# Optimization experiments

Measured on AMD Instinct MI355X. Metric: run time of the kernel, lower is better.

Reference implementation:

```python
import jax, jax.numpy as jnp
import numpy as np

# Static multi-scale feature map shapes (value_spatial_shapes) - constants for jit.
SPATIAL = [(128, 128), (64, 64), (32, 32), (16, 16)]
D = 256      # embed_dim
NH = 8       # num_heads
HD = D // NH # head_dim = 32
L = 4        # num_levels
P = 4        # num_points
TP = NH * L * P  # 128 total points


def setup_inputs() -> dict:
    key = jax.random.key(0)
    ks = jax.random.split(key, 10)
    bs, lq = 8, 300
    lv = sum(h * w for h, w in SPATIAL)  # 21760
    s = D ** -0.5
    return {
        "query": jax.random.normal(ks[0], (bs, lq, D), jnp.float32),
        "reference_points": jax.random.uniform(ks[1], (bs, lq, L, 4), jnp.float32),
        "value": jax.random.normal(ks[2], (bs, lv, D), jnp.float32),
        "W_value": jax.random.normal(ks[3], (D, D), jnp.float32) * s,
        "b_value": jnp.zeros((D,), jnp.float32),
        "W_off": jax.random.normal(ks[4], (D, TP * 2), jnp.float32) * (s * 0.01),
        "b_off": jax.random.normal(ks[5], (TP * 2,), jnp.float32) * 0.5,
        "W_attn": jax.random.normal(ks[6], (D, TP), jnp.float32) * (s * 0.01),
        "b_attn": jnp.zeros((TP,), jnp.float32),
        "W_out": jax.random.normal(ks[7], (D, D), jnp.float32) * s,
        "b_out": jnp.zeros((D,), jnp.float32),
    }


def _grid_sample(img, grid):
    """torch F.grid_sample(mode='bilinear', padding_mode='zeros', align_corners=False).
    img: [N, C, H, W]; grid: [N, Hg, Wg, 2] in [-1, 1] (x, y). Returns [N, C, Hg, Wg]."""
    N, C, H, W = img.shape
    gx = (grid[..., 0] + 1.0) * (W * 0.5) - 0.5
    gy = (grid[..., 1] + 1.0) * (H * 0.5) - 0.5
    x0f = jnp.floor(gx)
    y0f = jnp.floor(gy)
    x0 = x0f.astype(jnp.int32)
    y0 = y0f.astype(jnp.int32)
    x1, y1 = x0 + 1, y0 + 1
    wx1 = gx - x0f
    wy1 = gy - y0f
    wx0 = 1.0 - wx1
    wy0 = 1.0 - wy1
    imgf = img.reshape(N, C, H * W)

    def gather(ix, iy):
        valid = (ix >= 0) & (ix < W) & (iy >= 0) & (iy < H)
        idx = jnp.clip(iy, 0, H - 1) * W + jnp.clip(ix, 0, W - 1)
        v = jax.vmap(lambda im, ii: im[:, ii])(imgf, idx)  # [N, C, Hg, Wg]
        return v * valid[:, None, :, :].astype(img.dtype)

    return (gather(x0, y0) * (wx0 * wy0)[:, None]
            + gather(x1, y0) * (wx1 * wy0)[:, None]
            + gather(x0, y1) * (wx0 * wy1)[:, None]
            + gather(x1, y1) * (wx1 * wy1)[:, None])


def reference(query, reference_points, value, W_value, b_value, W_off, b_off,
              W_attn, b_attn, W_out, b_out):
    bs, lq, _ = query.shape
    # value projection + head split
    v = (value @ W_value + b_value).reshape(bs, -1, NH, HD)
    # sampling offsets and attention weights from query
    off = (query @ W_off + b_off).reshape(bs, lq, NH, L, P, 2)
    aw = jax.nn.softmax((query @ W_attn + b_attn).reshape(bs, lq, NH, L * P), axis=-1)
    aw = aw.reshape(bs, lq, NH, L, P)
    # reference_points last dim == 4 branch (cx, cy, w, h)
    ref = reference_points  # [bs, lq, L, 4]
    loc = ref[:, :, None, :, None, :2] + off / P * ref[:, :, None, :, None, 2:] * 0.5
    grids = 2.0 * loc - 1.0  # [bs, lq, NH, L, P, 2]
    # split value per level
    splits = np.cumsum([h * w for h, w in SPATIAL])[:-1]
    v_list = jnp.split(v, splits, axis=1)
    samples = []
    for l, (h, w) in enumerate(SPATIAL):
        img = v_list[l].transpose(0, 2, 3, 1).reshape(bs * NH, HD, h, w)
        g = grids[:, :, :, l].transpose(0, 2, 1, 3, 4).reshape(bs * NH, lq, P, 2)
        samples.append(_grid_sample(img, g))  # [bs*NH, HD, lq, P]
    samp = jnp.stack(samples, axis=-2).reshape(bs * NH, HD, lq, L * P)
    awr = aw.transpose(0, 2, 1, 3, 4).reshape(bs * NH, 1, lq, L * P)
    out = (samp * awr).sum(-1).reshape(bs, NH * HD, lq).transpose(0, 2, 1)
    return out @ W_out + b_out
```

## Files before the change

kernel.cpp:

```cpp
#include <hip/hip_runtime.h>
#include <hip/hip_bf16.h>

typedef short bf16x8 __attribute__((ext_vector_type(8)));
typedef unsigned short u16x8 __attribute__((ext_vector_type(8)));
typedef float f32x4 __attribute__((ext_vector_type(4)));

#define LQ 300
#define LV 21760
#define NQ 2400
#define MROWS 174080

#define VBM 32
#define VGRID 512
#define VNT (MROWS / VBM)

__device__ __forceinline__ unsigned short f2bf(float x) {
    __hip_bfloat16 h = __float2bfloat16(x);
    return *reinterpret_cast<unsigned short*>(&h);
}
__device__ __forceinline__ float bf2f(unsigned short s) {
    return __uint_as_float(((unsigned)s) << 16);
}
__device__ __forceinline__ bf16x8 cvt8(float4 a, float4 b) {
    u16x8 u;
    u[0] = f2bf(a.x); u[1] = f2bf(a.y); u[2] = f2bf(a.z); u[3] = f2bf(a.w);
    u[4] = f2bf(b.x); u[5] = f2bf(b.y); u[6] = f2bf(b.z); u[7] = f2bf(b.w);
    return (bf16x8)u;
}
__device__ __forceinline__ bf16x8 cvt8v(f32x4 a, f32x4 b) {
    u16x8 u;
    u[0] = f2bf(a[0]); u[1] = f2bf(a[1]); u[2] = f2bf(a[2]); u[3] = f2bf(a[3]);
    u[4] = f2bf(b[0]); u[5] = f2bf(b[1]); u[6] = f2bf(b[2]); u[7] = f2bf(b[3]);
    return (bf16x8)u;
}

__global__ void k_wt(const float* __restrict__ Wv, const float* __restrict__ Woff,
                     const float* __restrict__ Wattn, const float* __restrict__ Wout,
                     unsigned short* __restrict__ ws) {
    int i = blockIdx.x * 256 + threadIdx.x;
    if (i < 65536) {
        int n = i >> 8, k = i & 255;
        ws[i] = f2bf(Wv[k * 256 + n]);
    } else if (i < 65536 + 98304) {
        int j = i - 65536;
        int n = j >> 8, k = j & 255;
        float s = (n < 256) ? Woff[k * 256 + n] : Wattn[k * 128 + (n - 256)];
        ws[i] = f2bf(s);
    } else {
        int j = i - 163840;
        int n = j >> 8, k = j & 255;
        ws[i] = f2bf(Wout[k * 256 + n]);
    }
}

__global__ __launch_bounds__(256, 2) void k_vgemm(
    const float* __restrict__ A, const unsigned short* __restrict__ Bt,
    const float* __restrict__ bias, unsigned short* __restrict__ V)
{
    __shared__ __align__(16) float buf[2][VBM * 256];
    const int t = threadIdx.x;
    const int lane = t & 63;
    const int wv = t >> 6;
    const int fr = lane & 15, kg = lane >> 4;

    bf16x8 bw[8][4];
#pragma unroll
    for (int kk = 0; kk < 8; ++kk)
#pragma unroll
        for (int n = 0; n < 4; ++n)
            bw[kk][n] = *(const bf16x8*)(Bt + (size_t)(wv * 64 + n * 16 + fr) * 256 + kk * 32 + kg * 8);
    float bv[4];
#pragma unroll
    for (int n = 0; n < 4; ++n) bv[n] = bias[wv * 64 + n * 16 + fr];

#define VSTAGE(tile, cb)                                                                  \
    {                                                                                     \
        const char* tb = (const char*)(A + (size_t)(tile) * (VBM * 256));                 \
        _Pragma("unroll")                                                                 \
        for (int i = 0; i < 8; ++i) {                                                     \
            const int r = wv * 8 + i;                                                     \
            __builtin_amdgcn_global_load_lds(                                             \
                (const __attribute__((address_space(1))) void*)                           \
                    (tb + (size_t)r * 1024 + ((lane * 16) ^ ((r & 7) << 4))),             \
                (__attribute__((address_space(3))) void*)&buf[cb][r * 256], 16, 0, 0);    \
        }                                                                                 \
    }

    VSTAGE((int)blockIdx.x, 0);

    int cur = 0;
    for (int tile = blockIdx.x; tile < VNT; tile += VGRID, cur ^= 1) {
        const int nxt = tile + VGRID;
        const bool stged = (nxt < VNT);
        if (stged) VSTAGE(nxt, cur ^ 1);
        if (tile == (int)blockIdx.x) {
            if (stged) asm volatile("s_waitcnt vmcnt(8)" ::: "memory");
            else       asm volatile("s_waitcnt vmcnt(0)" ::: "memory");
        } else {
            if (stged) asm volatile("s_waitcnt vmcnt(12)" ::: "memory");
            else       asm volatile("s_waitcnt vmcnt(4)" ::: "memory");
        }
        __builtin_amdgcn_s_barrier();

        const float* lp = buf[cur];
        f32x4 acc[2][4];
#pragma unroll
        for (int m = 0; m < 2; ++m)
#pragma unroll
            for (int n = 0; n < 4; ++n) { f32x4 z = {0.f, 0.f, 0.f, 0.f}; acc[m][n] = z; }

#pragma unroll
        for (int kk = 0; kk < 8; ++kk) {
            bf16x8 a[2];
#pragma unroll
            for (int m = 0; m < 2; ++m) {
                const int row = m * 16 + fr;
                const int bsw = ((kk * 32 + kg * 8) * 4) ^ ((row & 7) << 4);
                f32x4 af0 = *(const f32x4*)((const char*)(lp + row * 256) + bsw);
                f32x4 af1 = *(const f32x4*)((const char*)(lp + row * 256) + (bsw ^ 16));
                a[m] = cvt8v(af0, af1);
            }
#pragma unroll
            for (int m = 0; m < 2; ++m)
#pragma unroll
                for (int n = 0; n < 4; ++n)
                    acc[m][n] = __builtin_amdgcn_mfma_f32_16x16x32_bf16(a[m], bw[kk][n], acc[m][n], 0, 0, 0);
        }

        __builtin_amdgcn_s_barrier();

        unsigned short* cp = (unsigned short*)buf[cur];
#pragma unroll
        for (int n = 0; n < 4; ++n)
#pragma unroll
            for (int m = 0; m < 2; ++m)
#pragma unroll
                for (int r = 0; r < 4; ++r)
                    cp[(m * 16 + kg * 4 + r) * 264 + wv * 64 + n * 16 + fr] =
                        f2bf(acc[m][n][r] + bv[n]);
        asm volatile("s_waitcnt lgkmcnt(0)" ::: "memory");
        __builtin_amdgcn_sched_barrier(0);
        __builtin_amdgcn_s_barrier();

        unsigned short* ob = V + (size_t)tile * (VBM * 256);
#pragma unroll
        for (int i = 0; i < 4; ++i) {
            const int f = i * 256 + t;
            const int row = f >> 5, col = (f & 31) * 8;
            *(u16x8*)(ob + row * 256 + col) = *(const u16x8*)&cp[row * 264 + col];
        }
        __builtin_amdgcn_s_barrier();
    }
#undef VSTAGE
}

__global__ __launch_bounds__(512) void k_qproj(
    const float* __restrict__ Q, const unsigned short* __restrict__ Woa,
    const float* __restrict__ b_off, const float* __restrict__ b_attn,
    float* __restrict__ offattn)
{
    const int t = threadIdx.x;
    const int lane = t & 63;
    const int wid = t >> 6;
    const int wr = wid >> 2, wc = wid & 3;
    const int fr = lane & 15, kg = lane >> 4;
    const int rowBase = blockIdx.x * 64;

    const int r0 = min(rowBase + wr * 32 + fr, NQ - 1);
    const int r1 = min(rowBase + wr * 32 + 16 + fr, NQ - 1);

    f32x4 acc[2][6];
#pragma unroll
    for (int m = 0; m < 2; m++)
#pragma unroll
        for (int n = 0; n < 6; n++) { f32x4 z = {0.f, 0.f, 0.f, 0.f}; acc[m][n] = z; }

#pragma unroll
    for (int kk = 0; kk < 8; ++kk) {
        const int kb = kk * 32 + kg * 8;
        float4 q00 = *(const float4*)(Q + (size_t)r0 * 256 + kb);
        float4 q01 = *(const float4*)(Q + (size_t)r0 * 256 + kb + 4);
        float4 q10 = *(const float4*)(Q + (size_t)r1 * 256 + kb);
        float4 q11 = *(const float4*)(Q + (size_t)r1 * 256 + kb + 4);
        bf16x8 a0 = cvt8(q00, q01);
        bf16x8 a1 = cvt8(q10, q11);
#pragma unroll
        for (int n = 0; n < 6; n++) {
            bf16x8 bb = *(const bf16x8*)(Woa + (size_t)(wc * 96 + n * 16 + fr) * 256 + kb);
            acc[0][n] = __builtin_amdgcn_mfma_f32_16x16x32_bf16(a0, bb, acc[0][n], 0, 0, 0);
            acc[1][n] = __builtin_amdgcn_mfma_f32_16x16x32_bf16(a1, bb, acc[1][n], 0, 0, 0);
        }
    }

#pragma unroll
    for (int m = 0; m < 2; m++) {
#pragma unroll
        for (int n = 0; n < 6; n++) {
            int col = wc * 96 + n * 16 + fr;
            float bvv = (col < 256) ? b_off[col] : b_attn[col - 256];
#pragma unroll
            for (int r = 0; r < 4; r++) {
                int row = rowBase + wr * 32 + m * 16 + kg * 4 + r;
                if (row < NQ) offattn[(size_t)row * 384 + col] = acc[m][n][r] + bvv;
            }
        }
    }
}

__global__ __launch_bounds__(256) void k_sample(
    const float* __restrict__ refp, const float* __restrict__ offattn,
    const unsigned short* __restrict__ V, unsigned short* __restrict__ att)
{
    __shared__ float aw[2][128], gx[2][128], gy[2][128];
    const int t = threadIdx.x;
    const int jj = t >> 7;
    const int tt = t & 127;
    const int row = blockIdx.x * 2 + jj;
    const int b = row / LQ;
    const float* oa = offattn + (size_t)row * 384;

    {
        float logit = oa[256 + tt];
        float m = logit;
        m = fmaxf(m, __shfl_xor(m, 1));
        m = fmaxf(m, __shfl_xor(m, 2));
        m = fmaxf(m, __shfl_xor(m, 4));
        m = fmaxf(m, __shfl_xor(m, 8));
        float e = __expf(logit - m);
        float s = e;
        s += __shfl_xor(s, 1);
        s += __shfl_xor(s, 2);
        s += __shfl_xor(s, 4);
        s += __shfl_xor(s, 8);
        aw[jj][tt] = e / s;
        const int l = (tt >> 2) & 3;
        const float Wl = (l == 0) ? 128.f : (l == 1) ? 64.f : (l == 2) ? 32.f : 16.f;
        float ox = oa[2 * tt], oy = oa[2 * tt + 1];
        const float* rp = refp + ((size_t)row * 4 + l) * 4;
        gx[jj][tt] = (rp[0] + ox * 0.125f * rp[2]) * Wl - 0.5f;
        gy[jj][tt] = (rp[1] + oy * 0.125f * rp[3]) * Wl - 0.5f;
    }
    __syncthreads();

    const int h = tt >> 4;
    const int ch = h * 32 + (tt & 15) * 2;
    float acc0 = 0.f, acc1 = 0.f;
#pragma unroll 4
    for (int p = 0; p < 16; p++) {
        const int l = p >> 2;
        const int Wl = (l == 0) ? 128 : (l == 1) ? 64 : (l == 2) ? 32 : 16;
        const int S  = (l == 0) ? 0 : (l == 1) ? 16384 : (l == 2) ? 20480 : 21504;
        int pt = h * 16 + p;
        float a  = aw[jj][pt];
        float sx = gx[jj][pt], sy = gy[jj][pt];
        float x0f = floorf(sx), y0f = floorf(sy);
        int   x0 = (int)x0f, y0 = (int)y0f;
        float wx1 = sx - x0f, wy1 = sy - y0f;
        float wx0 = 1.f - wx1, wy0 = 1.f - wy1;
        bool vx0 = (unsigned)x0 < (unsigned)Wl;
        bool vx1 = (unsigned)(x0 + 1) < (unsigned)Wl;
        bool vy0 = (unsigned)y0 < (unsigned)Wl;
        bool vy1 = (unsigned)(y0 + 1) < (unsigned)Wl;
        float p00x = 0.f, p00y = 0.f, p01x = 0.f, p01y = 0.f;
        float p10x = 0.f, p10y = 0.f, p11x = 0.f, p11y = 0.f;
        size_t pixBase = (size_t)b * LV + S;
        if (vy0) {
            size_t rb = (pixBase + (size_t)y0 * Wl) * 256 + ch;
            if (vx0) { unsigned u = *(const unsigned*)(V + rb + (size_t)x0 * 256);
                       p00x = bf2f((unsigned short)u); p00y = bf2f((unsigned short)(u >> 16)); }
            if (vx1) { unsigned u = *(const unsigned*)(V + rb + (size_t)x0 * 256 + 256);
                       p01x = bf2f((unsigned short)u); p01y = bf2f((unsigned short)(u >> 16)); }
        }
        if (vy1) {
            size_t rb = (pixBase + (size_t)(y0 + 1) * Wl) * 256 + ch;
            if (vx0) { unsigned u = *(const unsigned*)(V + rb + (size_t)x0 * 256);
                       p10x = bf2f((unsigned short)u); p10y = bf2f((unsigned short)(u >> 16)); }
            if (vx1) { unsigned u = *(const unsigned*)(V + rb + (size_t)x0 * 256 + 256);
                       p11x = bf2f((unsigned short)u); p11y = bf2f((unsigned short)(u >> 16)); }
        }
        acc0 += a * (wy0 * (wx0 * p00x + wx1 * p01x) + wy1 * (wx0 * p10x + wx1 * p11x));
        acc1 += a * (wy0 * (wx0 * p00y + wx1 * p01y) + wy1 * (wx0 * p10y + wx1 * p11y));
    }
    unsigned short o2[2] = { f2bf(acc0), f2bf(acc1) };
    *(unsigned*)(att + (size_t)row * 256 + ch) = *(const unsigned*)o2;
}

__global__ __launch_bounds__(256) void k_outproj(
    const unsigned short* __restrict__ att, const unsigned short* __restrict__ Wout,
    const float* __restrict__ b_out, float* __restrict__ out)
{
    const int t = threadIdx.x;
    const int lane = t & 63;
    const int wc = t >> 6;
    const int fr = lane & 15, kg = lane >> 4;
    const int rowBase = blockIdx.x * 64;

    f32x4 acc[4][4];
#pragma unroll
    for (int m = 0; m < 4; m++)
#pragma unroll
        for (int n = 0; n < 4; n++) { f32x4 z = {0.f, 0.f, 0.f, 0.f}; acc[m][n] = z; }

#pragma unroll
    for (int kk = 0; kk < 8; ++kk) {
        const int kb = kk * 32 + kg * 8;
        bf16x8 a[4], bb[4];
#pragma unroll
        for (int m = 0; m < 4; m++) {
            int row = min(rowBase + m * 16 + fr, NQ - 1);
            a[m] = *(const bf16x8*)(att + (size_t)row * 256 + kb);
        }
#pragma unroll
        for (int n = 0; n < 4; n++)
            bb[n] = *(const bf16x8*)(Wout + (size_t)(wc * 64 + n * 16 + fr) * 256 + kb);
#pragma unroll
        for (int m = 0; m < 4; m++)
#pragma unroll
            for (int n = 0; n < 4; n++)
                acc[m][n] = __builtin_amdgcn_mfma_f32_16x16x32_bf16(a[m], bb[n], acc[m][n], 0, 0, 0);
    }

#pragma unroll
    for (int m = 0; m < 4; m++) {
#pragma unroll
        for (int n = 0; n < 4; n++) {
            int col = wc * 64 + n * 16 + fr;
            float bvv = b_out[col];
#pragma unroll
            for (int r = 0; r < 4; r++) {
                int row = rowBase + m * 16 + kg * 4 + r;
                if (row < NQ) out[(size_t)row * 256 + col] = acc[m][n][r] + bvv;
            }
        }
    }
}

extern "C" void kernel_launch(void* const* d_in, const int* in_sizes, int n_in,
                              void* d_out, int out_size, void* d_ws, size_t ws_size,
                              hipStream_t stream) {
    const float* query   = (const float*)d_in[0];
    const float* refp    = (const float*)d_in[1];
    const float* value   = (const float*)d_in[2];
    const float* W_value = (const float*)d_in[3];
    const float* b_value = (const float*)d_in[4];
    const float* W_off   = (const float*)d_in[5];
    const float* b_off   = (const float*)d_in[6];
    const float* W_attn  = (const float*)d_in[7];
    const float* b_attn  = (const float*)d_in[8];
    const float* W_out   = (const float*)d_in[9];
    const float* b_out   = (const float*)d_in[10];
    float* out = (float*)d_out;

    unsigned short* wsu   = (unsigned short*)d_ws;
    unsigned short* Wt_v  = wsu;
    unsigned short* Wt_oa = Wt_v + 65536;
    unsigned short* Wt_out= Wt_oa + 98304;
    unsigned short* V     = Wt_out + 65536;
    float* offattn = (float*)(V + (size_t)MROWS * 256);
    unsigned short* att = (unsigned short*)(offattn + (size_t)NQ * 384);

    k_wt<<<896, 256, 0, stream>>>(W_value, W_off, W_attn, W_out, wsu);
    k_vgemm<<<VGRID, 256, 0, stream>>>(value, Wt_v, b_value, V);
    k_qproj<<<38, 512, 0, stream>>>(query, Wt_oa, b_off, b_attn, offattn);
    k_sample<<<NQ / 2, 256, 0, stream>>>(refp, offattn, V, att);
    k_outproj<<<38, 256, 0, stream>>>(att, Wt_out, b_out, out);
}
```

Before: 124.4 us.

## Fuse query projection into value GEMM launch and output projection into sampler

The query offset/attention projection now runs in 38 extra blocks of the value-GEMM kernel, so it overlaps with that kernel instead of needing its own launch. The output projection is folded into the sampling kernel: each block keeps its two sampled rows in shared memory and computes the 256 output columns with scalar FMAs against bf16 Wout. This drops two launches and the intermediate att buffer. In exchange, the output projection moves from MFMA to scalar math, and every sampling block re-reads the full 128KB Wout, roughly 1200 times.

```diff
diff --git a/kernel.cpp b/kernel.cpp
--- a/kernel.cpp
+++ b/kernel.cpp
@@ -12,6 +12,7 @@
 
 #define VBM 32
 #define VGRID 512
+#define QBLK 38
 #define VNT (MROWS / VBM)
 
 __device__ __forceinline__ unsigned short f2bf(float x) {
@@ -55,13 +56,63 @@
 
 __global__ __launch_bounds__(256, 2) void k_vgemm(
     const float* __restrict__ A, const unsigned short* __restrict__ Bt,
-    const float* __restrict__ bias, unsigned short* __restrict__ V)
+    const float* __restrict__ bias, unsigned short* __restrict__ V,
+    const float* __restrict__ Q, const unsigned short* __restrict__ Woa,
+    const float* __restrict__ b_off, const float* __restrict__ b_attn,
+    float* __restrict__ offattn)
 {
     __shared__ __align__(16) float buf[2][VBM * 256];
     const int t = threadIdx.x;
     const int lane = t & 63;
     const int wv = t >> 6;
     const int fr = lane & 15, kg = lane >> 4;
+
+    if (blockIdx.x < QBLK) {
+        const int rowBase = blockIdx.x * 64;
+        int rr[4];
+#pragma unroll
+        for (int m = 0; m < 4; ++m) rr[m] = min(rowBase + m * 16 + fr, NQ - 1);
+
+        f32x4 acc[4][6];
+#pragma unroll
+        for (int m = 0; m < 4; m++)
+#pragma unroll
+            for (int n = 0; n < 6; n++) { f32x4 z = {0.f, 0.f, 0.f, 0.f}; acc[m][n] = z; }
+
+#pragma unroll
+        for (int kk = 0; kk < 8; ++kk) {
+            const int kb = kk * 32 + kg * 8;
+            bf16x8 a[4];
+#pragma unroll
+            for (int m = 0; m < 4; ++m) {
+                float4 q0 = *(const float4*)(Q + (size_t)rr[m] * 256 + kb);
+                float4 q1 = *(const float4*)(Q + (size_t)rr[m] * 256 + kb + 4);
+                a[m] = cvt8(q0, q1);
+            }
+#pragma unroll
+            for (int n = 0; n < 6; n++) {
+                bf16x8 bb = *(const bf16x8*)(Woa + (size_t)(wv * 96 + n * 16 + fr) * 256 + kb);
+#pragma unroll
+                for (int m = 0; m < 4; ++m)
+                    acc[m][n] = __builtin_amdgcn_mfma_f32_16x16x32_bf16(a[m], bb, acc[m][n], 0, 0, 0);
+            }
+        }
+
+#pragma unroll
+        for (int m = 0; m < 4; m++) {
+#pragma unroll
+            for (int n = 0; n < 6; n++) {
+                int col = wv * 96 + n * 16 + fr;
+                float bvv = (col < 256) ? b_off[col] : b_attn[col - 256];
+#pragma unroll
+                for (int r = 0; r < 4; r++) {
+                    int row = rowBase + m * 16 + kg * 4 + r;
+                    if (row < NQ) offattn[(size_t)row * 384 + col] = acc[m][n][r] + bvv;
+                }
+            }
+        }
+        return;
+    }
 
     bf16x8 bw[8][4];
 #pragma unroll
@@ -86,14 +137,15 @@
         }                                                                                 \
     }
 
-    VSTAGE((int)blockIdx.x, 0);
+    const int tb0 = (int)blockIdx.x - QBLK;
+    VSTAGE(tb0, 0);
 
     int cur = 0;
-    for (int tile = blockIdx.x; tile < VNT; tile += VGRID, cur ^= 1) {
+    for (int tile = tb0; tile < VNT; tile += VGRID, cur ^= 1) {
         const int nxt = tile + VGRID;
         const bool stged = (nxt < VNT);
         if (stged) VSTAGE(nxt, cur ^ 1);
-        if (tile == (int)blockIdx.x) {
+        if (tile == tb0) {
             if (stged) asm volatile("s_waitcnt vmcnt(8)" ::: "memory");
             else       asm volatile("s_waitcnt vmcnt(0)" ::: "memory");
         } else {
@@ -154,64 +206,13 @@
 #undef VSTAGE
 }
 
-__global__ __launch_bounds__(512) void k_qproj(
-    const float* __restrict__ Q, const unsigned short* __restrict__ Woa,
-    const float* __restrict__ b_off, const float* __restrict__ b_attn,
-    float* __restrict__ offattn)
-{
-    const int t = threadIdx.x;
-    const int lane = t & 63;
-    const int wid = t >> 6;
-    const int wr = wid >> 2, wc = wid & 3;
-    const int fr = lane & 15, kg = lane >> 4;
-    const int rowBase = blockIdx.x * 64;
-
-    const int r0 = min(rowBase + wr * 32 + fr, NQ - 1);
-    const int r1 = min(rowBase + wr * 32 + 16 + fr, NQ - 1);
-
-    f32x4 acc[2][6];
-#pragma unroll
-    for (int m = 0; m < 2; m++)
-#pragma unroll
-        for (int n = 0; n < 6; n++) { f32x4 z = {0.f, 0.f, 0.f, 0.f}; acc[m][n] = z; }
-
-#pragma unroll
-    for (int kk = 0; kk < 8; ++kk) {
-        const int kb = kk * 32 + kg * 8;
-        float4 q00 = *(const float4*)(Q + (size_t)r0 * 256 + kb);
-        float4 q01 = *(const float4*)(Q + (size_t)r0 * 256 + kb + 4);
-        float4 q10 = *(const float4*)(Q + (size_t)r1 * 256 + kb);
-        float4 q11 = *(const float4*)(Q + (size_t)r1 * 256 + kb + 4);
-        bf16x8 a0 = cvt8(q00, q01);
-        bf16x8 a1 = cvt8(q10, q11);
-#pragma unroll
-        for (int n = 0; n < 6; n++) {
-            bf16x8 bb = *(const bf16x8*)(Woa + (size_t)(wc * 96 + n * 16 + fr) * 256 + kb);
-            acc[0][n] = __builtin_amdgcn_mfma_f32_16x16x32_bf16(a0, bb, acc[0][n], 0, 0, 0);
-            acc[1][n] = __builtin_amdgcn_mfma_f32_16x16x32_bf16(a1, bb, acc[1][n], 0, 0, 0);
-        }
-    }
-
-#pragma unroll
-    for (int m = 0; m < 2; m++) {
-#pragma unroll
-        for (int n = 0; n < 6; n++) {
-            int col = wc * 96 + n * 16 + fr;
-            float bvv = (col < 256) ? b_off[col] : b_attn[col - 256];
-#pragma unroll
-            for (int r = 0; r < 4; r++) {
-                int row = rowBase + wr * 32 + m * 16 + kg * 4 + r;
-                if (row < NQ) offattn[(size_t)row * 384 + col] = acc[m][n][r] + bvv;
-            }
-        }
-    }
-}
-
 __global__ __launch_bounds__(256) void k_sample(
     const float* __restrict__ refp, const float* __restrict__ offattn,
-    const unsigned short* __restrict__ V, unsigned short* __restrict__ att)
+    const unsigned short* __restrict__ V, const unsigned short* __restrict__ Wout,
+    const float* __restrict__ b_out, float* __restrict__ out)
 {
     __shared__ float aw[2][128], gx[2][128], gy[2][128];
+    __shared__ float att_s[2][256];
     const int t = threadIdx.x;
     const int jj = t >> 7;
     const int tt = t & 127;
@@ -281,58 +282,25 @@
         acc0 += a * (wy0 * (wx0 * p00x + wx1 * p01x) + wy1 * (wx0 * p10x + wx1 * p11x));
         acc1 += a * (wy0 * (wx0 * p00y + wx1 * p01y) + wy1 * (wx0 * p10y + wx1 * p11y));
     }
-    unsigned short o2[2] = { f2bf(acc0), f2bf(acc1) };
-    *(unsigned*)(att + (size_t)row * 256 + ch) = *(const unsigned*)o2;
-}
-
-__global__ __launch_bounds__(256) void k_outproj(
-    const unsigned short* __restrict__ att, const unsigned short* __restrict__ Wout,
-    const float* __restrict__ b_out, float* __restrict__ out)
-{
-    const int t = threadIdx.x;
-    const int lane = t & 63;
-    const int wc = t >> 6;
-    const int fr = lane & 15, kg = lane >> 4;
-    const int rowBase = blockIdx.x * 64;
-
-    f32x4 acc[4][4];
-#pragma unroll
-    for (int m = 0; m < 4; m++)
-#pragma unroll
-        for (int n = 0; n < 4; n++) { f32x4 z = {0.f, 0.f, 0.f, 0.f}; acc[m][n] = z; }
-
-#pragma unroll
-    for (int kk = 0; kk < 8; ++kk) {
-        const int kb = kk * 32 + kg * 8;
-        bf16x8 a[4], bb[4];
-#pragma unroll
-        for (int m = 0; m < 4; m++) {
-            int row = min(rowBase + m * 16 + fr, NQ - 1);
-            a[m] = *(const bf16x8*)(att + (size_t)row * 256 + kb);
-        }
-#pragma unroll
-        for (int n = 0; n < 4; n++)
-            bb[n] = *(const bf16x8*)(Wout + (size_t)(wc * 64 + n * 16 + fr) * 256 + kb);
-#pragma unroll
-        for (int m = 0; m < 4; m++)
-#pragma unroll
-            for (int n = 0; n < 4; n++)
-                acc[m][n] = __builtin_amdgcn_mfma_f32_16x16x32_bf16(a[m], bb[n], acc[m][n], 0, 0, 0);
-    }
-
-#pragma unroll
-    for (int m = 0; m < 4; m++) {
-#pragma unroll
-        for (int n = 0; n < 4; n++) {
-            int col = wc * 64 + n * 16 + fr;
-            float bvv = b_out[col];
-#pragma unroll
-            for (int r = 0; r < 4; r++) {
-                int row = rowBase + m * 16 + kg * 4 + r;
-                if (row < NQ) out[(size_t)row * 256 + col] = acc[m][n][r] + bvv;
-            }
-        }
-    }
+    att_s[jj][ch] = acc0;
+    att_s[jj][ch + 1] = acc1;
+    __syncthreads();
+
+    const size_t r0 = (size_t)blockIdx.x * 2;
+    float o0 = b_out[t], o1 = o0;
+    const unsigned short* wrow = Wout + (size_t)t * 256;
+#pragma unroll 8
+    for (int k = 0; k < 256; k += 8) {
+        bf16x8 w8 = *(const bf16x8*)(wrow + k);
+#pragma unroll
+        for (int e = 0; e < 8; ++e) {
+            float w = bf2f((unsigned short)w8[e]);
+            o0 += att_s[0][k + e] * w;
+            o1 += att_s[1][k + e] * w;
+        }
+    }
+    out[r0 * 256 + t] = o0;
+    out[(r0 + 1) * 256 + t] = o1;
 }
 
 extern "C" void kernel_launch(void* const* d_in, const int* in_sizes, int n_in,
@@ -357,11 +325,9 @@
     unsigned short* Wt_out= Wt_oa + 98304;
     unsigned short* V     = Wt_out + 65536;
     float* offattn = (float*)(V + (size_t)MROWS * 256);
-    unsigned short* att = (unsigned short*)(offattn + (size_t)NQ * 384);
 
     k_wt<<<896, 256, 0, stream>>>(W_value, W_off, W_attn, W_out, wsu);
-    k_vgemm<<<VGRID, 256, 0, stream>>>(value, Wt_v, b_value, V);
-    k_qproj<<<38, 512, 0, stream>>>(query, Wt_oa, b_off, b_attn, offattn);
-    k_sample<<<NQ / 2, 256, 0, stream>>>(refp, offattn, V, att);
-    k_outproj<<<38, 256, 0, stream>>>(att, Wt_out, b_out, out);
-}
+    k_vgemm<<<VGRID + QBLK, 256, 0, stream>>>(value, Wt_v, b_value, V,
+                                              query, Wt_oa, b_off, b_attn, offattn);
+    k_sample<<<NQ / 2, 256, 0, stream>>>(refp, offattn, V, Wt_out, b_out, out);
+}
```

Result: slower. 133.6 us (+7.5%).
